# Kernel optimization log

Hardware: AMD Instinct MI355X
Metric: run time of the kernel (lower is better)

Reference implementation:

```python
import jax, jax.numpy as jnp
import numpy as np

B = 64           # number of graphs
MAXN = 128       # max nodes per graph (== to_dense_batch n)
D = 512          # hidden_dim
H = 16           # n_attn_heads
HS = D // H      # head_size
SCALE = HS ** -0.5
EPS = 1e-5

# deterministic ragged node counts in [64,128], max exactly 128
_COUNTS = 64 + (np.arange(B) * 37) % 65
NTOT = int(_COUNTS.sum())  # 6148


def setup_inputs() -> dict:
    key = jax.random.key(0)
    ks = jax.random.split(key, 10)
    r = D ** -0.5  # uniform init radius used by the module

    def lin(k):
        kw, kb = jax.random.split(k)
        W = jax.random.uniform(kw, (D, D), minval=-r, maxval=r, dtype=jnp.float32)
        b = jax.random.uniform(kb, (D,), minval=-r, maxval=r, dtype=jnp.float32)
        return W, b

    Wq, bq = lin(ks[0])
    Wk, bk = lin(ks[1])
    Wv, bv = lin(ks[2])
    Wp, bp = lin(ks[3])
    x = jax.random.normal(ks[4], (NTOT, D), dtype=jnp.float32)
    attn_bias = 0.1 * jax.random.normal(ks[5], (B, H, MAXN, MAXN), dtype=jnp.float32)
    batch = jnp.asarray(np.repeat(np.arange(B), _COUNTS), dtype=jnp.int32)
    return {
        "x": x, "attn_bias": attn_bias,
        "Wq": Wq, "bq": bq, "Wk": Wk, "bk": bk, "Wv": Wv, "bv": bv,
        "Wp": Wp, "bp": bp,
        "ln_w": jnp.ones((D,), jnp.float32), "ln_b": jnp.zeros((D,), jnp.float32),
        "batch": batch,
    }


def reference(x, attn_bias, Wq, bq, Wk, bk, Wv, bv, Wp, bp, ln_w, ln_b, batch):
    # eval-mode BiasedSelfAttentionLayer (all dropouts are identity)
    Bn, Hh, n, _ = attn_bias.shape
    N = x.shape[0]
    # to_dense_batch: per-node position inside its graph
    counts = jax.ops.segment_sum(jnp.ones(N, jnp.int32), batch, num_segments=Bn)
    starts = jnp.cumsum(counts) - counts
    pos = jnp.arange(N) - starts[batch]
    x_dense = jnp.zeros((Bn, n, D), x.dtype).at[batch, pos].set(x)  # [B,n,D]
    mask = jnp.zeros((Bn, n), bool).at[batch, pos].set(True)        # [B,n]

    def heads(W, b):
        return (x_dense @ W.T + b).reshape(Bn, n, Hh, HS).transpose(0, 2, 1, 3)

    q = heads(Wq, bq)  # [B,H,n,hs]
    k = heads(Wk, bk)
    v = heads(Wv, bv)

    attn = jnp.einsum("bhqd,bhkd->bhqk", q, k) * SCALE + attn_bias  # [B,H,n,n]
    mask2 = mask[:, None, :, None]  # valid queries
    mask3 = mask[:, None, None, :]  # valid keys
    attn = jnp.where(mask3, attn, -jnp.inf)   # masked_fill(~mask3, -inf)
    attn = jnp.where(mask2, attn, 0.0)        # masked_fill(~mask2, 0.0)
    attn = jax.nn.softmax(attn, axis=-1)
    attn = jnp.where(mask2, attn, 0.0)        # re-zero invalid query rows

    out = jnp.einsum("bhqk,bhkd->bhqd", attn, v)           # [B,H,n,hs]
    out = out.transpose(0, 2, 1, 3).reshape(Bn, n, D)      # [B,n,D]
    out = out @ Wp.T + bp
    out = out[batch, pos] + x                               # scatter back + residual
    # LayerNorm
    mu = out.mean(-1, keepdims=True)
    var = out.var(-1, keepdims=True)
    return (out - mu) / jnp.sqrt(var + EPS) * ln_w + ln_b
```

## Files before the change

### kernel.cpp

```cpp
#include <hip/hip_runtime.h>
#include <math.h>

#define NTOT 6148
#define NB 64
#define DM 512
#define SCALE_F 0.17677669529663687f

typedef __attribute__((ext_vector_type(8))) short bf16x8;
typedef __attribute__((ext_vector_type(4))) float f32x4;

__device__ __forceinline__ short f2bf(float f) {
  union { float f; unsigned u; } v; v.f = f;
  unsigned r = (v.u + 0x7fffu + ((v.u >> 16) & 1u)) >> 16;
  return (short)r;
}

__device__ __forceinline__ void gl_lds16(const void* g, void* l) {
  auto gp = (const __attribute__((address_space(1))) unsigned*)(unsigned long long)(uintptr_t)g;
  auto lp = (__attribute__((address_space(3))) unsigned*)(unsigned long long)(uintptr_t)l;
  __builtin_amdgcn_global_load_lds(gp, lp, 16, 0, 0);
}

__global__ __launch_bounds__(256) void k_starts(const int* __restrict__ batch,
                                                int* __restrict__ starts) {
  int i = blockIdx.x * 256 + threadIdx.x;
  if (i >= NTOT) return;
  int b = batch[i];
  if (i == 0) starts[b] = 0;
  else if (batch[i - 1] != b) starts[b] = i;
  if (i == NTOT - 1) starts[NB] = NTOT;
}

__global__ __launch_bounds__(256) void k_cvt(const float* __restrict__ x,
                                             const float* __restrict__ wq,
                                             const float* __restrict__ wk,
                                             const float* __restrict__ wv,
                                             const float* __restrict__ wp,
                                             short* __restrict__ xb,
                                             short* __restrict__ wqb,
                                             short* __restrict__ wkb,
                                             short* __restrict__ wvb,
                                             short* __restrict__ wpb) {
  const int bid = blockIdx.x;
  const float* s; short* d; long off;
  if (bid < 1537) {
    s = x; d = xb;
    off = ((long)bid * 256 + threadIdx.x) * 8;
  } else {
    int wi = (bid - 1537) >> 7;
    s = (wi == 0) ? wq : (wi == 1) ? wk : (wi == 2) ? wv : wp;
    d = (wi == 0) ? wqb : (wi == 1) ? wkb : (wi == 2) ? wvb : wpb;
    off = ((long)((bid - 1537) & 127) * 256 + threadIdx.x) * 8;
  }
  float4 v0 = *(const float4*)(s + off);
  float4 v1 = *(const float4*)(s + off + 4);
  bf16x8 o;
  o[0] = f2bf(v0.x); o[1] = f2bf(v0.y); o[2] = f2bf(v0.z); o[3] = f2bf(v0.w);
  o[4] = f2bf(v1.x); o[5] = f2bf(v1.y); o[6] = f2bf(v1.z); o[7] = f2bf(v1.w);
  *(bf16x8*)(d + off) = o;
}

template <int NT, bool BF16OUT>
__global__ __launch_bounds__(256) void k_gemm_mfma(
    const short* __restrict__ Abf,
    const short* __restrict__ W0, const short* __restrict__ W1, const short* __restrict__ W2,
    const float* __restrict__ b0, const float* __restrict__ b1, const float* __restrict__ b2,
    const float* __restrict__ resid, void* __restrict__ Cv, int ldc, int M) {
  constexpr int NF = NT / 32;
  __shared__ __align__(16) short As[2][64][32];
  __shared__ __align__(16) short Bs[2][NT][32];
  const int tid = threadIdx.x;
  const int w = tid >> 6, l = tid & 63;
  const int m0 = blockIdx.y * 64;
  const int n0 = blockIdx.x * NT;
  const int sel = n0 >> 9;
  const short* Wt = (sel == 0) ? W0 : (sel == 1) ? W1 : W2;
  const float* bt = (sel == 0) ? b0 : (sel == 1) ? b1 : b2;
  const int nl0 = n0 & 511;
  const int wr = w >> 1, wc = w & 1;
  const int lr = l >> 2;
  const int lc = (l & 3) * 8;
  const int fr = l & 15, fs = (l >> 4) * 8;

  const long gaA = (long)min(m0 + w * 16 + lr, M - 1) * 512 + lc;
  const long gaB0 = (long)(nl0 + ((NT == 128) ? w * 32 : w * 16) + lr) * 512 + lc;
  const long gaB1 = (long)(nl0 + w * 32 + 16 + lr) * 512 + lc;

  f32x4 acc[2][NF];
#pragma unroll
  for (int m = 0; m < 2; m++)
#pragma unroll
    for (int n = 0; n < NF; n++) acc[m][n] = (f32x4){0.f, 0.f, 0.f, 0.f};

  auto stage = [&](int kt, int buf) {
    const int k0 = kt * 32;
    gl_lds16(Abf + gaA + k0, &As[buf][w * 16][0]);
    if (NT == 128) {
      gl_lds16(Wt + gaB0 + k0, &Bs[buf][w * 32][0]);
      gl_lds16(Wt + gaB1 + k0, &Bs[buf][w * 32 + 16][0]);
    } else {
      gl_lds16(Wt + gaB0 + k0, &Bs[buf][w * 16][0]);
    }
  };
  auto compute = [&](int buf) {
    bf16x8 af[2], bfr[NF];
#pragma unroll
    for (int m = 0; m < 2; m++) af[m] = *(const bf16x8*)&As[buf][wr * 32 + m * 16 + fr][fs];
#pragma unroll
    for (int n = 0; n < NF; n++)
      bfr[n] = *(const bf16x8*)&Bs[buf][wc * (NT / 2) + n * 16 + fr][fs];
#pragma unroll
    for (int m = 0; m < 2; m++)
#pragma unroll
      for (int n = 0; n < NF; n++)
        acc[m][n] = __builtin_amdgcn_mfma_f32_16x16x32_bf16(af[m], bfr[n], acc[m][n], 0, 0, 0);
  };

  stage(0, 0);
  __syncthreads();
  for (int step = 0; step < 16; step++) {
    if (step < 15) stage(step + 1, (step + 1) & 1);
    compute(step & 1);
    __syncthreads();
  }

  const int er = (l >> 4) * 4, ec = l & 15;
#pragma unroll
  for (int n = 0; n < NF; n++) {
    const int col = n0 + wc * (NT / 2) + n * 16 + ec;
    const float bv = bt[col & 511];
#pragma unroll
    for (int m = 0; m < 2; m++) {
      const int rowb = m0 + wr * 32 + m * 16 + er;
#pragma unroll
      for (int j = 0; j < 4; j++) {
        const int row = rowb + j;
        if (row < M) {
          float v = acc[m][n][j] + bv;
          if (resid) v += resid[(long)row * 512 + col];
          if (BF16OUT) ((short*)Cv)[(long)row * ldc + col] = f2bf(v);
          else ((float*)Cv)[(long)row * ldc + col] = v;
        }
      }
    }
  }
}

__global__ __launch_bounds__(256, 3) void k_attn(const short* __restrict__ QKVbf,
                                                 const float* __restrict__ bias,
                                                 const int* __restrict__ starts,
                                                 short* __restrict__ Obf) {
  __shared__ __align__(16) float BiasP[4][8][264];
  __shared__ __align__(16) short Vtb[32][136];
  const int id = blockIdx.x;
  const int wg = (id & 7) * 256 + (id >> 3);
  const int b = wg >> 5, qc = (wg >> 4) & 1, h = wg & 15;
  const int tid = threadIdx.x, l = tid & 63, w = tid >> 6;
  const int wq0 = qc * 64 + w * 16;
  const int lg = l >> 4, lk = l & 15, fs = lg * 8;
  short* Pw = (short*)&BiasP[w][0][0];

  const int s0 = starts[b], cnt = starts[b + 1] - s0;
  const bool active = wq0 < cnt;

  const int u = l >> 2, c = (l & 3) * 8;
  const int vr0 = w * 32 + u, vr1 = vr0 + 16;
  const short* vbase = QKVbf + 1024 + h * 32 + c;
  const bf16x8 v0 = *(const bf16x8*)(vbase + (long)(s0 + min(vr0, cnt - 1)) * 1536);
  const bf16x8 v1 = *(const bf16x8*)(vbase + (long)(s0 + min(vr1, cnt - 1)) * 1536);

  bf16x8 aq, bk[8];
  if (active) {
    const short* qbase = QKVbf + h * 32 + fs;
    aq = *(const bf16x8*)(qbase + (long)(s0 + min(wq0 + lk, cnt - 1)) * 1536);
#pragma unroll
    for (int n = 0; n < 8; n++)
      bk[n] = *(const bf16x8*)(qbase + 512 + (long)(s0 + min(n * 16 + lk, cnt - 1)) * 1536);
    const float* bsrc = bias + ((long)(b * 16 + h) << 14) + (long)wq0 * 128 + l * 4;
#pragma unroll
    for (int t = 0; t < 8; t++)
      gl_lds16(bsrc + t * 256, &BiasP[w][t][0]);
  }

#pragma unroll
  for (int i = 0; i < 8; i++) Vtb[c + i][vr0] = v0[i];
#pragma unroll
  for (int i = 0; i < 8; i++) Vtb[c + i][vr1] = v1[i];

  f32x4 S[8];
  float invs[4];
  if (active) {
#pragma unroll
    for (int n = 0; n < 8; n++)
      S[n] = __builtin_amdgcn_mfma_f32_16x16x32_bf16(aq, bk[n],
                                                     (f32x4){0.f, 0.f, 0.f, 0.f}, 0, 0, 0);
    asm volatile("s_waitcnt vmcnt(0)" ::: "memory");
    __builtin_amdgcn_sched_barrier(0);

#pragma unroll
    for (int n = 0; n < 8; n++) {
      const int k = n * 16 + lk;
      const bool kok = k < cnt;
#pragma unroll
      for (int j = 0; j < 4; j++) {
        const int r = lg * 4 + j;
        const float sv = S[n][j] * SCALE_F + BiasP[w][r >> 1][(r & 1) * 128 + k];
        S[n][j] = kok ? sv : -1e30f;
      }
    }
#pragma unroll
    for (int j = 0; j < 4; j++) {
      float mx = S[0][j];
#pragma unroll
      for (int n = 1; n < 8; n++) mx = fmaxf(mx, S[n][j]);
      mx = fmaxf(mx, __shfl_xor(mx, 1));
      mx = fmaxf(mx, __shfl_xor(mx, 2));
      mx = fmaxf(mx, __shfl_xor(mx, 4));
      mx = fmaxf(mx, __shfl_xor(mx, 8));
      float sum = 0.f;
#pragma unroll
      for (int n = 0; n < 8; n++) {
        const float p = __expf(S[n][j] - mx);
        S[n][j] = p;
        sum += p;
      }
      sum += __shfl_xor(sum, 1);
      sum += __shfl_xor(sum, 2);
      sum += __shfl_xor(sum, 4);
      sum += __shfl_xor(sum, 8);
      invs[j] = 1.f / sum;
      const int r = lg * 4 + j;
#pragma unroll
      for (int n = 0; n < 8; n++) Pw[r * 136 + n * 16 + lk] = f2bf(S[n][j]);
    }
  }

  __syncthreads();
  if (!active) return;

  f32x4 O[2];
#pragma unroll
  for (int dt = 0; dt < 2; dt++) O[dt] = (f32x4){0.f, 0.f, 0.f, 0.f};
#pragma unroll
  for (int kc = 0; kc < 4; kc++) {
    const bf16x8 pa = *(const bf16x8*)&Pw[lk * 136 + kc * 32 + fs];
#pragma unroll
    for (int dt = 0; dt < 2; dt++) {
      const bf16x8 vb = *(const bf16x8*)&Vtb[dt * 16 + lk][kc * 32 + fs];
      O[dt] = __builtin_amdgcn_mfma_f32_16x16x32_bf16(pa, vb, O[dt], 0, 0, 0);
    }
  }
#pragma unroll
  for (int j = 0; j < 4; j++) {
    const int q = wq0 + lg * 4 + j;
    if (q < cnt) {
      short* orow = Obf + (long)(s0 + q) * 512 + h * 32;
#pragma unroll
      for (int dt = 0; dt < 2; dt++)
        orow[dt * 16 + lk] = f2bf(O[dt][j] * invs[j]);
    }
  }
}

__global__ __launch_bounds__(256) void k_lnp(const float* __restrict__ pre,
                                             const float* __restrict__ lw,
                                             const float* __restrict__ lb,
                                             float* __restrict__ out) {
  const int row = blockIdx.x * 4 + (threadIdx.x >> 6);
  if (row >= NTOT) return;
  const int lane = threadIdx.x & 63;
  const float* pr = pre + (long)row * 512 + lane * 8;
  float4 p0 = *(const float4*)pr;
  float4 p1 = *(const float4*)(pr + 4);
  float v[8] = {p0.x, p0.y, p0.z, p0.w, p1.x, p1.y, p1.z, p1.w};
  float s = 0.f, s2 = 0.f;
#pragma unroll
  for (int j = 0; j < 8; j++) { s += v[j]; s2 += v[j] * v[j]; }
#pragma unroll
  for (int off = 32; off > 0; off >>= 1) {
    s += __shfl_xor(s, off);
    s2 += __shfl_xor(s2, off);
  }
  const float mu = s * (1.f / 512.f);
  const float var = s2 * (1.f / 512.f) - mu * mu;
  const float inv = rsqrtf(var + 1e-5f);
  float4 w0 = *(const float4*)&lw[lane * 8];
  float4 w1 = *(const float4*)&lw[lane * 8 + 4];
  float4 b0 = *(const float4*)&lb[lane * 8];
  float4 b1 = *(const float4*)&lb[lane * 8 + 4];
  float4 o0 = make_float4((v[0] - mu) * inv * w0.x + b0.x, (v[1] - mu) * inv * w0.y + b0.y,
                          (v[2] - mu) * inv * w0.z + b0.z, (v[3] - mu) * inv * w0.w + b0.w);
  float4 o1 = make_float4((v[4] - mu) * inv * w1.x + b1.x, (v[5] - mu) * inv * w1.y + b1.y,
                          (v[6] - mu) * inv * w1.z + b1.z, (v[7] - mu) * inv * w1.w + b1.w);
  float* dst = out + (long)row * 512 + lane * 8;
  *(float4*)dst = o0;
  *(float4*)(dst + 4) = o1;
}

extern "C" void kernel_launch(void* const* d_in, const int* in_sizes, int n_in,
                              void* d_out, int out_size, void* d_ws, size_t ws_size,
                              hipStream_t stream) {
  const float* x = (const float*)d_in[0];
  const float* attn_bias = (const float*)d_in[1];
  const float* Wq = (const float*)d_in[2];
  const float* bq = (const float*)d_in[3];
  const float* Wk = (const float*)d_in[4];
  const float* bk = (const float*)d_in[5];
  const float* Wv = (const float*)d_in[6];
  const float* bv = (const float*)d_in[7];
  const float* Wp = (const float*)d_in[8];
  const float* bp = (const float*)d_in[9];
  const float* ln_w = (const float*)d_in[10];
  const float* ln_b = (const float*)d_in[11];
  const int* batch = (const int*)d_in[12];
  float* out = (float*)d_out;

  char* ws = (char*)d_ws;
  int* starts = (int*)ws;
  short* Xbf = (short*)(ws + 512);
  short* Wqb = Xbf + (long)NTOT * 512;
  short* Wkb = Wqb + 512 * 512;
  short* Wvb = Wkb + 512 * 512;
  short* Wpb = Wvb + 512 * 512;
  short* QKVbf = Wpb + 512 * 512;
  short* Obf = Xbf;
  float* proj = (float*)QKVbf;

  k_starts<<<(NTOT + 255) / 256, 256, 0, stream>>>(batch, starts);
  k_cvt<<<1537 + 4 * 128, 256, 0, stream>>>(x, Wq, Wk, Wv, Wp, Xbf, Wqb, Wkb, Wvb, Wpb);

  dim3 gq(12, (NTOT + 63) / 64);
  k_gemm_mfma<128, true><<<gq, 256, 0, stream>>>(Xbf, Wqb, Wkb, Wvb, bq, bk, bv,
                                                 nullptr, QKVbf, 1536, NTOT);

  k_attn<<<2048, 256, 0, stream>>>(QKVbf, attn_bias, starts, Obf);

  dim3 gp(8, (NTOT + 63) / 64);
  k_gemm_mfma<64, false><<<gp, 256, 0, stream>>>(Obf, Wpb, Wpb, Wpb, bp, bp, bp,
                                                 x, proj, 512, NTOT);

  k_lnp<<<(NTOT + 3) / 4, 256, 0, stream>>>(proj, ln_w, ln_b, out);
}
```

Measured before the change: 81.47 us.

## Fuse starts computation into convert kernel and load attention bias into registers

The separate k_starts launch is folded into the first 25 blocks of the conversion kernel, removing one kernel launch. In the attention kernel, the bias tile is now loaded straight from global memory into registers in MFMA output layout instead of async-copied into LDS, so LDS shrinks to a bf16 P buffer. The explicit vmcnt wait is dropped. This adds 32 float registers per thread, and the occupancy hint drops from 3 to 2 blocks per CU. The per-lane global loads are 16-lane contiguous 4-byte accesses, which may coalesce less well than the 16-byte LDS copies.

```diff
diff --git a/kernel.cpp b/kernel.cpp
--- a/kernel.cpp
+++ b/kernel.cpp
@@ -19,16 +19,6 @@
   auto gp = (const __attribute__((address_space(1))) unsigned*)(unsigned long long)(uintptr_t)g;
   auto lp = (__attribute__((address_space(3))) unsigned*)(unsigned long long)(uintptr_t)l;
   __builtin_amdgcn_global_load_lds(gp, lp, 16, 0, 0);
-}
-
-__global__ __launch_bounds__(256) void k_starts(const int* __restrict__ batch,
-                                                int* __restrict__ starts) {
-  int i = blockIdx.x * 256 + threadIdx.x;
-  if (i >= NTOT) return;
-  int b = batch[i];
-  if (i == 0) starts[b] = 0;
-  else if (batch[i - 1] != b) starts[b] = i;
-  if (i == NTOT - 1) starts[NB] = NTOT;
 }
 
 __global__ __launch_bounds__(256) void k_cvt(const float* __restrict__ x,
@@ -40,8 +30,19 @@
                                              short* __restrict__ wqb,
                                              short* __restrict__ wkb,
                                              short* __restrict__ wvb,
-                                             short* __restrict__ wpb) {
+                                             short* __restrict__ wpb,
+                                             const int* __restrict__ batch,
+                                             int* __restrict__ starts) {
   const int bid = blockIdx.x;
+  if (bid < 25) {
+    const int i = bid * 256 + threadIdx.x;
+    if (i < NTOT) {
+      const int bb = batch[i];
+      if (i == 0) starts[bb] = 0;
+      else if (batch[i - 1] != bb) starts[bb] = i;
+      if (i == NTOT - 1) starts[NB] = NTOT;
+    }
+  }
   const float* s; short* d; long off;
   if (bid < 1537) {
     s = x; d = xb;
@@ -146,11 +147,11 @@
   }
 }
 
-__global__ __launch_bounds__(256, 3) void k_attn(const short* __restrict__ QKVbf,
+__global__ __launch_bounds__(256, 2) void k_attn(const short* __restrict__ QKVbf,
                                                  const float* __restrict__ bias,
                                                  const int* __restrict__ starts,
                                                  short* __restrict__ Obf) {
-  __shared__ __align__(16) float BiasP[4][8][264];
+  __shared__ __align__(16) short Ps[4][16][136];
   __shared__ __align__(16) short Vtb[32][136];
   const int id = blockIdx.x;
   const int wg = (id & 7) * 256 + (id >> 3);
@@ -158,7 +159,6 @@
   const int tid = threadIdx.x, l = tid & 63, w = tid >> 6;
   const int wq0 = qc * 64 + w * 16;
   const int lg = l >> 4, lk = l & 15, fs = lg * 8;
-  short* Pw = (short*)&BiasP[w][0][0];
 
   const int s0 = starts[b], cnt = starts[b + 1] - s0;
   const bool active = wq0 < cnt;
@@ -170,16 +170,18 @@
   const bf16x8 v1 = *(const bf16x8*)(vbase + (long)(s0 + min(vr1, cnt - 1)) * 1536);
 
   bf16x8 aq, bk[8];
+  float bv[8][4];
   if (active) {
     const short* qbase = QKVbf + h * 32 + fs;
     aq = *(const bf16x8*)(qbase + (long)(s0 + min(wq0 + lk, cnt - 1)) * 1536);
 #pragma unroll
     for (int n = 0; n < 8; n++)
       bk[n] = *(const bf16x8*)(qbase + 512 + (long)(s0 + min(n * 16 + lk, cnt - 1)) * 1536);
-    const float* bsrc = bias + ((long)(b * 16 + h) << 14) + (long)wq0 * 128 + l * 4;
-#pragma unroll
-    for (int t = 0; t < 8; t++)
-      gl_lds16(bsrc + t * 256, &BiasP[w][t][0]);
+    const float* bb = bias + ((long)(b * 16 + h) << 14) + (long)(wq0 + lg * 4) * 128 + lk;
+#pragma unroll
+    for (int n = 0; n < 8; n++)
+#pragma unroll
+      for (int j = 0; j < 4; j++) bv[n][j] = bb[j * 128 + n * 16];
   }
 
 #pragma unroll
@@ -187,24 +189,20 @@
 #pragma unroll
   for (int i = 0; i < 8; i++) Vtb[c + i][vr1] = v1[i];
 
-  f32x4 S[8];
   float invs[4];
   if (active) {
+    f32x4 S[8];
 #pragma unroll
     for (int n = 0; n < 8; n++)
       S[n] = __builtin_amdgcn_mfma_f32_16x16x32_bf16(aq, bk[n],
                                                      (f32x4){0.f, 0.f, 0.f, 0.f}, 0, 0, 0);
-    asm volatile("s_waitcnt vmcnt(0)" ::: "memory");
-    __builtin_amdgcn_sched_barrier(0);
-
 #pragma unroll
     for (int n = 0; n < 8; n++) {
       const int k = n * 16 + lk;
       const bool kok = k < cnt;
 #pragma unroll
       for (int j = 0; j < 4; j++) {
-        const int r = lg * 4 + j;
-        const float sv = S[n][j] * SCALE_F + BiasP[w][r >> 1][(r & 1) * 128 + k];
+        const float sv = S[n][j] * SCALE_F + bv[n][j];
         S[n][j] = kok ? sv : -1e30f;
       }
     }
@@ -231,7 +229,7 @@
       invs[j] = 1.f / sum;
       const int r = lg * 4 + j;
 #pragma unroll
-      for (int n = 0; n < 8; n++) Pw[r * 136 + n * 16 + lk] = f2bf(S[n][j]);
+      for (int n = 0; n < 8; n++) Ps[w][r][n * 16 + lk] = f2bf(S[n][j]);
     }
   }
 
@@ -243,7 +241,7 @@
   for (int dt = 0; dt < 2; dt++) O[dt] = (f32x4){0.f, 0.f, 0.f, 0.f};
 #pragma unroll
   for (int kc = 0; kc < 4; kc++) {
-    const bf16x8 pa = *(const bf16x8*)&Pw[lk * 136 + kc * 32 + fs];
+    const bf16x8 pa = *(const bf16x8*)&Ps[w][lk][kc * 32 + fs];
 #pragma unroll
     for (int dt = 0; dt < 2; dt++) {
       const bf16x8 vb = *(const bf16x8*)&Vtb[dt * 16 + lk][kc * 32 + fs];
@@ -326,8 +324,8 @@
   short* Obf = Xbf;
   float* proj = (float*)QKVbf;
 
-  k_starts<<<(NTOT + 255) / 256, 256, 0, stream>>>(batch, starts);
-  k_cvt<<<1537 + 4 * 128, 256, 0, stream>>>(x, Wq, Wk, Wv, Wp, Xbf, Wqb, Wkb, Wvb, Wpb);
+  k_cvt<<<1537 + 4 * 128, 256, 0, stream>>>(x, Wq, Wk, Wv, Wp, Xbf, Wqb, Wkb, Wvb, Wpb,
+                                            batch, starts);
 
   dim3 gq(12, (NTOT + 63) / 64);
   k_gemm_mfma<128, true><<<gq, 256, 0, stream>>>(Xbf, Wqb, Wkb, Wvb, bq, bk, bv,
```

After: 75.60 us (median of 2 runs). -7.2%, faster.
